# Performance work log

Measured on AMD Instinct MI355X. Metric: run time of the kernel, lower is better.

## Reference

```python
import jax, jax.numpy as jnp
import numpy as np

NEG_SLOPE = 0.2


def gat_layer(x, src, dst, W, a_src, a_dst, b, heads, ch, concat, n_nodes):
    # x: [N, F_in], W: [F_in, heads*ch]
    h = (x @ W).reshape(n_nodes, heads, ch)              # [N, H, C]
    alpha_src = jnp.sum(h * a_src, axis=-1)              # [N, H]
    alpha_dst = jnp.sum(h * a_dst, axis=-1)              # [N, H]
    e = jax.nn.leaky_relu(alpha_src[src] + alpha_dst[dst], NEG_SLOPE)  # [E, H]
    # segment softmax over edges grouped by destination node
    e_max = jax.ops.segment_max(e, dst, num_segments=n_nodes)          # [N, H]
    ex = jnp.exp(e - e_max[dst])                                       # [E, H]
    denom = jax.ops.segment_sum(ex, dst, num_segments=n_nodes)         # [N, H]
    alpha = ex / denom[dst]                                            # [E, H]
    msg = h[src] * alpha[:, :, None]                                   # [E, H, C]
    out = jax.ops.segment_sum(msg, dst, num_segments=n_nodes)          # [N, H, C]
    if concat:
        out = out.reshape(n_nodes, heads * ch)
    else:
        out = out.mean(axis=1)
    return out + b


def setup_inputs() -> dict:
    key = jax.random.key(0)
    ks = jax.random.split(key, 16)
    N, E, F_in = 50000, 800000, 128
    H, C, OUT = 4, 32, 64
    x = jax.random.normal(ks[0], (N, F_in), dtype=jnp.float32)
    edge_index = jax.random.randint(ks[1], (2, E), 0, N, dtype=jnp.int64)
    s = 0.1
    return {
        "x": x,
        "edge_index": edge_index,
        "W1": jax.random.normal(ks[2], (F_in, H * C), dtype=jnp.float32) * s,
        "a_src1": jax.random.normal(ks[3], (H, C), dtype=jnp.float32) * s,
        "a_dst1": jax.random.normal(ks[4], (H, C), dtype=jnp.float32) * s,
        "b1": jnp.zeros((H * C,), dtype=jnp.float32),
        "W2": jax.random.normal(ks[5], (H * C, H * C), dtype=jnp.float32) * s,
        "a_src2": jax.random.normal(ks[6], (H, C), dtype=jnp.float32) * s,
        "a_dst2": jax.random.normal(ks[7], (H, C), dtype=jnp.float32) * s,
        "b2": jnp.zeros((H * C,), dtype=jnp.float32),
        "W3": jax.random.normal(ks[8], (H * C, H * OUT), dtype=jnp.float32) * s,
        "a_src3": jax.random.normal(ks[9], (H, OUT), dtype=jnp.float32) * s,
        "a_dst3": jax.random.normal(ks[10], (H, OUT), dtype=jnp.float32) * s,
        "b3": jnp.zeros((OUT,), dtype=jnp.float32),
    }


def reference(x, edge_index, W1, a_src1, a_dst1, b1, W2, a_src2, a_dst2, b2,
              W3, a_src3, a_dst3, b3):
    N = x.shape[0]
    # PyG GATConv default add_self_loops=True
    loop = jnp.arange(N, dtype=edge_index.dtype)
    src = jnp.concatenate([edge_index[0], loop])
    dst = jnp.concatenate([edge_index[1], loop])
    h = gat_layer(x, src, dst, W1, a_src1, a_dst1, b1, 4, 32, True, N)
    h = gat_layer(h, src, dst, W2, a_src2, a_dst2, b2, 4, 32, True, N)
    out = gat_layer(h, src, dst, W3, a_src3, a_dst3, b3, 4, 64, False, N)
    return out
```

## Files before the change

### kernel.cpp

```cpp
#include <hip/hip_runtime.h>
#include <hip/hip_fp16.h>

constexpr int HEADS = 4;

typedef _Float16 half8 __attribute__((ext_vector_type(8)));
typedef _Float16 half2v __attribute__((ext_vector_type(2)));
typedef float f32x4 __attribute__((ext_vector_type(4)));

__device__ __forceinline__ float lrelu(float x) { return x > 0.f ? x : 0.2f * x; }


__global__ void count_deg_kernel(const int* __restrict__ ei, int* __restrict__ deg,
                                 int E, int N) {
  int e = blockIdx.x * 256 + threadIdx.x;
  int EP = E + N;
  if (e < EP) {
    int d = (e < E) ? ei[E + e] : (e - E);
    atomicAdd(&deg[d], 1);
  }
}

__global__ void scan_block_kernel(const int* __restrict__ deg, int* __restrict__ rowp,
                                  int* __restrict__ partials, int N) {
  __shared__ int sm[1024];
  int t = threadIdx.x;
  int i = blockIdx.x * 1024 + t;
  int v = (i < N) ? deg[i] : 0;
  sm[t] = v;
  __syncthreads();
  for (int off = 1; off < 1024; off <<= 1) {
    int tmp = (t >= off) ? sm[t - off] : 0;
    __syncthreads();
    sm[t] += tmp;
    __syncthreads();
  }
  if (i < N) rowp[i] = sm[t] - v;
  if (t == 1023) partials[blockIdx.x] = sm[t];
}

__global__ void scan_partials_kernel(int* partials, int nb) {
  __shared__ int sm[1024];
  int t = threadIdx.x;
  int v = (t < nb) ? partials[t] : 0;
  sm[t] = v;
  __syncthreads();
  for (int off = 1; off < 1024; off <<= 1) {
    int tmp = (t >= off) ? sm[t - off] : 0;
    __syncthreads();
    sm[t] += tmp;
    __syncthreads();
  }
  if (t < nb) partials[t] = sm[t] - v;
}

__global__ void add_off_kernel(int* __restrict__ rowp, const int* __restrict__ partials,
                               int N, int EP) {
  int i = blockIdx.x * 256 + threadIdx.x;
  if (i < N) rowp[i] += partials[i >> 10];
  if (i == 0) rowp[N] = EP;
}

__global__ void scatter_kernel(const int* __restrict__ ei, const int* __restrict__ rowp,
                               int* __restrict__ cursor, int* __restrict__ col,
                               int E, int N) {
  int e = blockIdx.x * 256 + threadIdx.x;
  int EP = E + N;
  if (e < EP) {
    int s, d;
    if (e < E) { s = ei[e]; d = ei[E + e]; }
    else       { s = e - E; d = e - E; }
    int pos = rowp[d] + atomicAdd(&cursor[d], 1);
    col[pos] = s;
  }
}


__global__ void convert_wt3_kernel(const float* __restrict__ W1, _Float16* __restrict__ Wt1,
                                   const float* __restrict__ W2, _Float16* __restrict__ Wt2,
                                   const float* __restrict__ W3, _Float16* __restrict__ Wt3) {
  const float* W; _Float16* Wt; int Fout;
  if (blockIdx.y == 0)      { W = W1; Wt = Wt1; Fout = 128; }
  else if (blockIdx.y == 1) { W = W2; Wt = Wt2; Fout = 128; }
  else                      { W = W3; Wt = Wt3; Fout = 256; }
  int i = blockIdx.x * 256 + threadIdx.x;
  if (i < 128 * Fout) {
    int c = i >> 7, k = i & 127;
    Wt[c * 128 + k] = (_Float16)W[k * Fout + c];
  }
}


template <int AF32, int CPH>
__global__ __launch_bounds__(256) void gemm_mfma_kernel(
    const void* __restrict__ Xv, const _Float16* __restrict__ Wt,
    const float* __restrict__ a_s, const float* __restrict__ a_d,
    _Float16* __restrict__ O, float* __restrict__ asrc, float* __restrict__ adst,
    int N, int Fout) {
  const int w = threadIdx.x >> 6;
  const int lane = threadIdx.x & 63;
  const int r = lane & 15, g = lane >> 4;
  const int row0 = blockIdx.x * 64 + w * 16;
  const int colpan = blockIdx.y * 128;

  int rowl = row0 + r;
  if (rowl >= N) rowl = N - 1;

  f32x4 acc[8];
#pragma unroll
  for (int c = 0; c < 8; ++c) acc[c] = {0.f, 0.f, 0.f, 0.f};

#pragma unroll
  for (int s = 0; s < 4; ++s) {
    half8 a;
    if constexpr (AF32) {
      const float* X = (const float*)Xv;
      float4 a0 = *(const float4*)&X[(size_t)rowl * 128 + s * 32 + g * 8];
      float4 a1 = *(const float4*)&X[(size_t)rowl * 128 + s * 32 + g * 8 + 4];
      a = half8{(_Float16)a0.x, (_Float16)a0.y, (_Float16)a0.z, (_Float16)a0.w,
                (_Float16)a1.x, (_Float16)a1.y, (_Float16)a1.z, (_Float16)a1.w};
    } else {
      const _Float16* X = (const _Float16*)Xv;
      a = *(const half8*)&X[(size_t)rowl * 128 + s * 32 + g * 8];
    }
#pragma unroll
    for (int c = 0; c < 8; ++c) {
      half8 b = *(const half8*)&Wt[(size_t)(colpan + c * 16 + r) * 128 + s * 32 + g * 8];
      acc[c] = __builtin_amdgcn_mfma_f32_16x16x32_f16(a, b, acc[c], 0, 0, 0);
    }
  }

#pragma unroll
  for (int c = 0; c < 8; ++c) {
    int ocol = colpan + c * 16 + r;
#pragma unroll
    for (int q = 0; q < 4; ++q) {
      int orow = row0 + g * 4 + q;
      if (orow < N) O[(size_t)orow * Fout + ocol] = (_Float16)acc[c][q];
    }
  }

  constexpr int HPP = 8 / CPH;
  constexpr int C = CPH * 16;
  const int hbase = blockIdx.y * HPP;
  float ps[4][HPP], pd[4][HPP];
#pragma unroll
  for (int q = 0; q < 4; ++q)
#pragma unroll
    for (int hh = 0; hh < HPP; ++hh) { ps[q][hh] = 0.f; pd[q][hh] = 0.f; }

#pragma unroll
  for (int c = 0; c < 8; ++c) {
    int hh = c / CPH;
    int ch = (c % CPH) * 16 + r;
    float asv = a_s[(hbase + hh) * C + ch];
    float adv = a_d[(hbase + hh) * C + ch];
#pragma unroll
    for (int q = 0; q < 4; ++q) {
      ps[q][hh] += acc[c][q] * asv;
      pd[q][hh] += acc[c][q] * adv;
    }
  }
#pragma unroll
  for (int m = 1; m < 16; m <<= 1) {
#pragma unroll
    for (int q = 0; q < 4; ++q)
#pragma unroll
      for (int hh = 0; hh < HPP; ++hh) {
        ps[q][hh] += __shfl_xor(ps[q][hh], m, 64);
        pd[q][hh] += __shfl_xor(pd[q][hh], m, 64);
      }
  }
  if (r == 0) {
#pragma unroll
    for (int q = 0; q < 4; ++q) {
      int row = row0 + g * 4 + q;
      if (row < N) {
#pragma unroll
        for (int hh = 0; hh < HPP; ++hh) {
          asrc[row * 4 + hbase + hh] = ps[q][hh];
          adst[row * 4 + hbase + hh] = pd[q][hh];
        }
      }
    }
  }
}


__global__ __launch_bounds__(256) void aggregate_concat_kernel(
    const _Float16* __restrict__ H, const float* __restrict__ asrc,
    const float* __restrict__ adst, const float* __restrict__ bias,
    const int* __restrict__ rowp, const int* __restrict__ col,
    _Float16* __restrict__ out, int N) {
  int n = blockIdx.x * 4 + (threadIdx.x >> 6);
  if (n >= N) return;
  int lane = threadIdx.x & 63;
  int h = lane >> 4;
  float ad = adst[n * 4 + h];
  int j = rowp[n], end = rowp[n + 1];
  float ax = 0.f, ay = 0.f, denom = 0.f;
  for (; j + 7 < end; j += 8) {
    int s[8]; float w[8]; half2v f[8];
#pragma unroll
    for (int k = 0; k < 8; ++k) s[k] = col[j + k];
#pragma unroll
    for (int k = 0; k < 8; ++k) {
      w[k] = __expf(lrelu(asrc[s[k] * 4 + h] + ad));
      f[k] = *(const half2v*)&H[(size_t)s[k] * 128 + lane * 2];
    }
#pragma unroll
    for (int k = 0; k < 8; ++k) {
      denom += w[k];
      ax += w[k] * (float)f[k].x;
      ay += w[k] * (float)f[k].y;
    }
  }
  for (; j < end; ++j) {
    int s0 = col[j];
    float w0 = __expf(lrelu(asrc[s0 * 4 + h] + ad));
    half2v f0 = *(const half2v*)&H[(size_t)s0 * 128 + lane * 2];
    denom += w0;
    ax += w0 * (float)f0.x;
    ay += w0 * (float)f0.y;
  }
  float inv = 1.f / denom;
  half2v o;
  o.x = (_Float16)(ax * inv + bias[lane * 2]);
  o.y = (_Float16)(ay * inv + bias[lane * 2 + 1]);
  *(half2v*)&out[(size_t)n * 128 + lane * 2] = o;
}


__global__ __launch_bounds__(128) void aggregate_mean_kernel(
    const _Float16* __restrict__ H, const float* __restrict__ asrc,
    const float* __restrict__ adst, const float* __restrict__ bias,
    const int* __restrict__ rowp, const int* __restrict__ col,
    float* __restrict__ out, int N) {
  __shared__ float2 red[128];
  int n = blockIdx.x;
  int t = threadIdx.x;
  int h = t >> 5;
  float ad = adst[n * 4 + h];
  int j = rowp[n], end = rowp[n + 1];
  float ax = 0.f, ay = 0.f, denom = 0.f;
  for (; j + 7 < end; j += 8) {
    int s[8]; float w[8]; half2v f[8];
#pragma unroll
    for (int k = 0; k < 8; ++k) s[k] = col[j + k];
#pragma unroll
    for (int k = 0; k < 8; ++k) {
      w[k] = __expf(lrelu(asrc[s[k] * 4 + h] + ad));
      f[k] = *(const half2v*)&H[(size_t)s[k] * 256 + t * 2];
    }
#pragma unroll
    for (int k = 0; k < 8; ++k) {
      denom += w[k];
      ax += w[k] * (float)f[k].x;
      ay += w[k] * (float)f[k].y;
    }
  }
  for (; j < end; ++j) {
    int s0 = col[j];
    float w0 = __expf(lrelu(asrc[s0 * 4 + h] + ad));
    half2v f0 = *(const half2v*)&H[(size_t)s0 * 256 + t * 2];
    denom += w0;
    ax += w0 * (float)f0.x;
    ay += w0 * (float)f0.y;
  }
  float inv = 1.f / denom;
  red[t] = make_float2(ax * inv, ay * inv);
  __syncthreads();
  if (t < 32) {
    float2 r0 = red[t], r1 = red[t + 32], r2 = red[t + 64], r3 = red[t + 96];
    float2 o = make_float2(0.25f * (r0.x + r1.x + r2.x + r3.x) + bias[t * 2],
                           0.25f * (r0.y + r1.y + r2.y + r3.y) + bias[t * 2 + 1]);
    *(float2*)&out[n * 64 + t * 2] = o;
  }
}


extern "C" void kernel_launch(void* const* d_in, const int* in_sizes, int n_in,
                              void* d_out, int out_size, void* d_ws, size_t ws_size,
                              hipStream_t stream) {
  const float* x   = (const float*)d_in[0];
  const int*   ei  = (const int*)d_in[1];
  const float* W1  = (const float*)d_in[2];
  const float* as1 = (const float*)d_in[3];
  const float* ad1 = (const float*)d_in[4];
  const float* b1  = (const float*)d_in[5];
  const float* W2  = (const float*)d_in[6];
  const float* as2 = (const float*)d_in[7];
  const float* ad2 = (const float*)d_in[8];
  const float* b2  = (const float*)d_in[9];
  const float* W3  = (const float*)d_in[10];
  const float* as3 = (const float*)d_in[11];
  const float* ad3 = (const float*)d_in[12];
  const float* b3  = (const float*)d_in[13];
  float* out = (float*)d_out;

  const int N  = in_sizes[0] / 128;
  const int E  = in_sizes[1] / 2;
  const int EP = E + N;

  char* p = (char*)d_ws;
  auto carve = [&](size_t bytes) -> void* {
    void* r = (void*)p;
    p += (bytes + 255) & ~size_t(255);
    return r;
  };
  int*      deg  = (int*)carve(size_t(N) * 4);
  int*      rowp = (int*)carve(size_t(N + 1) * 4);
  int*      cur  = (int*)carve(size_t(N) * 4);
  int*      part = (int*)carve(1024 * 4);
  int*      col  = (int*)carve(size_t(EP) * 4);
  float*    asrc = (float*)carve(size_t(N) * HEADS * 4);
  float*    adst = (float*)carve(size_t(N) * HEADS * 4);
  _Float16* Wt1  = (_Float16*)carve(128 * 128 * 2);
  _Float16* Wt2  = (_Float16*)carve(128 * 128 * 2);
  _Float16* Wt3  = (_Float16*)carve(256 * 128 * 2);
  _Float16* Hb   = (_Float16*)carve(size_t(N) * 256 * 2);
  _Float16* Ab   = (_Float16*)carve(size_t(N) * 128 * 2);

  hipMemsetAsync(deg, 0, size_t(N) * 4, stream);
  hipMemsetAsync(cur, 0, size_t(N) * 4, stream);

  int gEP = (EP + 255) / 256;
  count_deg_kernel<<<gEP, 256, 0, stream>>>(ei, deg, E, N);
  int nb = (N + 1023) / 1024;
  scan_block_kernel<<<nb, 1024, 0, stream>>>(deg, rowp, part, N);
  scan_partials_kernel<<<1, 1024, 0, stream>>>(part, nb);
  add_off_kernel<<<(N + 256) / 256, 256, 0, stream>>>(rowp, part, N, EP);
  scatter_kernel<<<gEP, 256, 0, stream>>>(ei, rowp, cur, col, E, N);

  convert_wt3_kernel<<<dim3(128, 3), 256, 0, stream>>>(W1, Wt1, W2, Wt2, W3, Wt3);

  int gM = (N + 63) / 64;
  int gN4 = (N + 3) / 4;

  gemm_mfma_kernel<1, 2><<<dim3(gM, 1), 256, 0, stream>>>(
      x, Wt1, as1, ad1, Hb, asrc, adst, N, 128);
  aggregate_concat_kernel<<<gN4, 256, 0, stream>>>(Hb, asrc, adst, b1, rowp, col, Ab, N);
  gemm_mfma_kernel<0, 2><<<dim3(gM, 1), 256, 0, stream>>>(
      Ab, Wt2, as2, ad2, Hb, asrc, adst, N, 128);
  aggregate_concat_kernel<<<gN4, 256, 0, stream>>>(Hb, asrc, adst, b2, rowp, col, Ab, N);
  gemm_mfma_kernel<0, 4><<<dim3(gM, 2), 256, 0, stream>>>(
      Ab, Wt3, as3, ad3, Hb, asrc, adst, N, 256);
  aggregate_mean_kernel<<<N, 128, 0, stream>>>(Hb, asrc, adst, b3, rowp, col, out, N);
}
```

Measured before the change: 422.5 us.

## Stage GEMM weights in swizzled LDS and share edge weights via shuffles

The MFMA GEMM kernel now copies its 128-column weight panel into a 32KB XOR-swizzled shared-memory tile once per block, so the inner MFMA loop reads B operands from LDS instead of global memory. The two aggregation kernels compute each 8-edge batch's attention weights (exp of leaky-relu) on 8 lanes per head group and broadcast them with __shfl, instead of every lane doing the asrc gather and exp itself. The cost is an extra LDS fill plus barrier per GEMM block, which may lower occupancy, and a shuffle-dependency chain in aggregation.

```diff
diff --git a/kernel.cpp b/kernel.cpp
--- a/kernel.cpp
+++ b/kernel.cpp
@@ -96,11 +96,24 @@
     const float* __restrict__ a_s, const float* __restrict__ a_d,
     _Float16* __restrict__ O, float* __restrict__ asrc, float* __restrict__ adst,
     int N, int Fout) {
-  const int w = threadIdx.x >> 6;
-  const int lane = threadIdx.x & 63;
+  __shared__ __align__(16) char Bl[32768];
+  const int t = threadIdx.x;
+  const int w = t >> 6;
+  const int lane = t & 63;
   const int r = lane & 15, g = lane >> 4;
   const int row0 = blockIdx.x * 64 + w * 16;
   const int colpan = blockIdx.y * 128;
+
+#pragma unroll
+  for (int i = 0; i < 8; ++i) {
+    int lin = i * 256 + t;
+    int c0 = lin >> 4;
+    int kb = lin & 15;
+    half8 v = *(const half8*)&Wt[(size_t)(colpan + c0) * 128 + kb * 8];
+    int addr = (c0 * 256 + kb * 16) ^ ((c0 & 7) << 4);
+    *(half8*)(Bl + addr) = v;
+  }
+  __syncthreads();
 
   int rowl = row0 + r;
   if (rowl >= N) rowl = N - 1;
@@ -124,7 +137,9 @@
     }
 #pragma unroll
     for (int c = 0; c < 8; ++c) {
-      half8 b = *(const half8*)&Wt[(size_t)(colpan + c * 16 + r) * 128 + s * 32 + g * 8];
+      int colr = c * 16 + r;
+      int addr = (colr * 256 + s * 64 + g * 16) ^ ((colr & 7) << 4);
+      half8 b = *(const half8*)(Bl + addr);
       acc[c] = __builtin_amdgcn_mfma_f32_16x16x32_f16(a, b, acc[c], 0, 0, 0);
     }
   }
@@ -197,21 +212,28 @@
   int h = lane >> 4;
   float ad = adst[n * 4 + h];
   int j = rowp[n], end = rowp[n + 1];
+  const bool comp = (lane & 15) < 8;
+  const int bsrc = lane & 48;
   float ax = 0.f, ay = 0.f, denom = 0.f;
   for (; j + 7 < end; j += 8) {
-    int s[8]; float w[8]; half2v f[8];
+    float wpre = 0.f;
+    if (comp) {
+      int sc = col[j + (lane & 7)];
+      wpre = __expf(lrelu(asrc[sc * 4 + h] + ad));
+    }
+    int s[8]; half2v f[8]; float wk[8];
 #pragma unroll
     for (int k = 0; k < 8; ++k) s[k] = col[j + k];
 #pragma unroll
     for (int k = 0; k < 8; ++k) {
-      w[k] = __expf(lrelu(asrc[s[k] * 4 + h] + ad));
+      wk[k] = __shfl(wpre, bsrc | k, 64);
       f[k] = *(const half2v*)&H[(size_t)s[k] * 128 + lane * 2];
     }
 #pragma unroll
     for (int k = 0; k < 8; ++k) {
-      denom += w[k];
-      ax += w[k] * (float)f[k].x;
-      ay += w[k] * (float)f[k].y;
+      denom += wk[k];
+      ax += wk[k] * (float)f[k].x;
+      ay += wk[k] * (float)f[k].y;
     }
   }
   for (; j < end; ++j) {
@@ -239,23 +261,31 @@
   int n = blockIdx.x;
   int t = threadIdx.x;
   int h = t >> 5;
+  int lane = t & 63;
   float ad = adst[n * 4 + h];
   int j = rowp[n], end = rowp[n + 1];
+  const bool comp = (lane & 31) < 8;
+  const int bsrc = lane & 32;
   float ax = 0.f, ay = 0.f, denom = 0.f;
   for (; j + 7 < end; j += 8) {
-    int s[8]; float w[8]; half2v f[8];
+    float wpre = 0.f;
+    if (comp) {
+      int sc = col[j + (lane & 7)];
+      wpre = __expf(lrelu(asrc[sc * 4 + h] + ad));
+    }
+    int s[8]; half2v f[8]; float wk[8];
 #pragma unroll
     for (int k = 0; k < 8; ++k) s[k] = col[j + k];
 #pragma unroll
     for (int k = 0; k < 8; ++k) {
-      w[k] = __expf(lrelu(asrc[s[k] * 4 + h] + ad));
+      wk[k] = __shfl(wpre, bsrc | k, 64);
       f[k] = *(const half2v*)&H[(size_t)s[k] * 256 + t * 2];
     }
 #pragma unroll
     for (int k = 0; k < 8; ++k) {
-      denom += w[k];
-      ax += w[k] * (float)f[k].x;
-      ay += w[k] * (float)f[k].y;
+      denom += wk[k];
+      ax += wk[k] * (float)f[k].x;
+      ay += wk[k] * (float)f[k].y;
     }
   }
   for (; j < end; ++j) {
```

Measured after the change: 406.2 us. 1.04x faster.
